# Kernel tuning notes

Measured on AMD Instinct MI355X. Metric: run time of the kernel, lower is better.

Reference implementation:

```python
import jax, jax.numpy as jnp
import numpy as np

B, T, C, H, D, S = 4096, 256, 64, 16, 16, 10


def setup_inputs() -> dict:
    key = jax.random.key(0)
    ks = jax.random.split(key, 8)
    return {
        'states_seq': jax.random.uniform(ks[0], (B, T, S), dtype=jnp.float32) + 0.5,
        'covariates_seq': jax.random.normal(ks[1], (B, T, C), dtype=jnp.float32),
        'ln_gamma': jnp.ones((C,), jnp.float32),
        'ln_beta': jnp.zeros((C,), jnp.float32),
        'rnn_wx': jax.random.normal(ks[2], (C, H), dtype=jnp.float32) * 0.1,
        'rnn_wh': jax.random.normal(ks[3], (H, H), dtype=jnp.float32) * 0.1,
        'rnn_b': jnp.zeros((H,), jnp.float32),
        'd1_w': jax.random.normal(ks[4], (H, H), dtype=jnp.float32) * 0.1,
        'd1_b': jnp.zeros((H,), jnp.float32),
        'd2_w': jax.random.normal(ks[5], (H, D), dtype=jnp.float32) * 0.1,
        'd2_b': jnp.zeros((D,), jnp.float32),
    }


def _cash_budget(s, d):
    # Deterministic cash-budget accounting update.
    # s: (B, 10) = [rev_prev, cash, AR, inventory, PPE, AP, debt, equity, retained, other]
    # d: (B, 16) drivers; first 10 used as ratios.
    sig = jax.nn.sigmoid
    g      = jnp.tanh(d[:, 0]) * 0.2      # sales growth
    cogs_m = sig(d[:, 1])                 # COGS margin
    opex_m = sig(d[:, 2]) * 0.5           # opex margin
    dep_r  = sig(d[:, 3]) * 0.1           # depreciation rate on PPE
    capex_r = sig(d[:, 4]) * 0.2          # capex as % of revenue
    dso = sig(d[:, 5])                    # AR ratio
    dio = sig(d[:, 6])                    # inventory ratio
    dpo = sig(d[:, 7])                    # AP ratio
    tax_r = sig(d[:, 8]) * 0.35           # tax rate
    int_r = sig(d[:, 9]) * 0.1            # interest rate on debt

    rev_prev, cash, ar, inv, ppe, ap, debt, equity, re, other = [s[:, i] for i in range(10)]
    rev = rev_prev * (1.0 + g)
    cogs = cogs_m * rev
    opex = opex_m * rev
    dep = dep_r * ppe
    interest = int_r * debt
    ebt = rev - cogs - opex - dep - interest
    tax = tax_r * jnp.maximum(ebt, 0.0)
    ni = ebt - tax
    ar_new = dso * rev
    inv_new = dio * cogs
    ap_new = dpo * cogs
    capex = capex_r * rev
    ppe_new = ppe + capex - dep
    cash_new = cash + ni + dep - capex - (ar_new - ar) - (inv_new - inv) + (ap_new - ap)
    re_new = re + ni
    s_next = jnp.stack([rev, cash_new, ar_new, inv_new, ppe_new, ap_new, debt, equity, re_new, other], axis=-1)
    is_out = jnp.stack([rev, cogs, opex, dep, interest, tax, ni], axis=-1)  # (B, 7)
    return s_next, is_out


def reference(states_seq, covariates_seq, ln_gamma, ln_beta, rnn_wx, rnn_wh, rnn_b, d1_w, d1_b, d2_w, d2_b):
    # LayerNormalization (keras default eps=1e-3, last axis)
    mu = covariates_seq.mean(-1, keepdims=True)
    var = covariates_seq.var(-1, keepdims=True)
    x = (covariates_seq - mu) * jax.lax.rsqrt(var + 1e-3) * ln_gamma + ln_beta

    # SimpleRNN: h_t = tanh(x_t Wx + h_{t-1} Wh + b), return_sequences
    xw = jnp.einsum('btc,ch->bth', x, rnn_wx) + rnn_b  # precompute input projection

    def rnn_step(h, xt):
        h = jnp.tanh(xt + h @ rnn_wh)
        return h, h

    h0 = jnp.zeros((x.shape[0], rnn_wh.shape[0]), x.dtype)
    _, hs = jax.lax.scan(rnn_step, h0, jnp.swapaxes(xw, 0, 1))  # (T, B, H)
    hs = jnp.swapaxes(hs, 0, 1)  # (B, T, H)

    drivers = jnp.tanh(hs @ d1_w + d1_b) @ d2_w + d2_b  # (B, T, D)

    # Cash-budget recurrence over t = 1 .. T-1
    def cb_step(s_prev, d_t):
        s_next, is_out = _cash_budget(s_prev, d_t)
        return s_next, (s_next, is_out)

    s0 = states_seq[:, 0, :]
    _, (states_tm, is_tm) = jax.lax.scan(cb_step, s0, jnp.swapaxes(drivers[:, 1:, :], 0, 1))
    states_pred = jnp.swapaxes(states_tm, 0, 1)  # (B, T-1, 10)
    is_pred = jnp.swapaxes(is_tm, 0, 1)          # (B, T-1, 7)
    return states_pred, is_pred
```

## Files before the change

kernel.cpp:

```cpp
#include <hip/hip_runtime.h>

#define NB 4096
#define NT 256
#define NC 64
#define NH 16
#define NS 10
#define NTO 255

__device__ __forceinline__ float fast_rcp(float x){
#if __has_builtin(__builtin_amdgcn_rcpf)
    return __builtin_amdgcn_rcpf(x);
#else
    return 1.0f/x;
#endif
}
__device__ __forceinline__ float fast_rsq(float x){
#if __has_builtin(__builtin_amdgcn_rsqf)
    return __builtin_amdgcn_rsqf(x);
#else
    return rsqrtf(x);
#endif
}
__device__ __forceinline__ float fsig(float x){
    return fast_rcp(1.0f + __expf(-x));
}
__device__ __forceinline__ float ftanh(float x){
    float e = __expf(2.0f*x);
    return fmaf(-2.0f, fast_rcp(e + 1.0f), 1.0f);
}

__global__ __launch_bounds__(64, 1) void vpf_kernel(
    const float* __restrict__ states, const float* __restrict__ cov,
    const float* __restrict__ lng,    const float* __restrict__ lnb,
    const float* __restrict__ wx,     const float* __restrict__ wh,
    const float* __restrict__ rnb,    const float* __restrict__ d1w,
    const float* __restrict__ d1b,    const float* __restrict__ d2w,
    const float* __restrict__ d2b,    float* __restrict__ out)
{
    const int lane = threadIdx.x;
    const int g = lane >> 4, l = lane & 15;
    const int b = (blockIdx.x << 2) + g;

    __shared__ __align__(16) float buf[2][4*NC];

    float gw[NC]; float Gs = 0.f, bacc = 0.f;
    #pragma unroll
    for (int c = 0; c < NC; ++c) {
        float w = wx[c*NH + l];
        float t = lng[c] * w;
        gw[c] = t; Gs += t;
        bacc = fmaf(lnb[c], w, bacc);
    }
    const float bwb = bacc + rnb[l];
    float whc[NH], d1c[NH], d2c[NH];
    #pragma unroll
    for (int k = 0; k < NH; ++k) {
        whc[k] = wh[k*NH + l];
        d1c[k] = d1w[k*NH + l];
        d2c[k] = d2w[k*NH + l];
    }
    const float d1bl = d1b[l], d2bl = d2b[l];

    float s0,s1,s2,s3,s4,s5,s6,s7,s8,s9;
    { const float* sp = states + (size_t)b*NT*NS;
      s0=sp[0];s1=sp[1];s2=sp[2];s3=sp[3];s4=sp[4];
      s5=sp[5];s6=sp[6];s7=sp[7];s8=sp[8];s9=sp[9]; }

    float* spo = out + (size_t)b*NTO*NS + l;
    float* ipo = out + (size_t)NB*NTO*NS + (size_t)b*NTO*7 + l;

    const float4* gp = (const float4*)(cov + (size_t)b*NT*NC) + l;
    float4 v0 = gp[0];
    float4 v1 = gp[16];
    float4 ra = gp[32];
    float4 rb = gp[48];
    ((float4*)buf[0])[lane] = v0;
    ((float4*)buf[1])[lane] = v1;
    __syncthreads();

    auto compute_xw = [&](const float* bp) -> float {
        const float4* row = (const float4*)(bp + g*NC);
        float4 ov = row[l];
        float ss = (ov.x+ov.y)+(ov.z+ov.w);
        float sq = fmaf(ov.x,ov.x, fmaf(ov.y,ov.y, fmaf(ov.z,ov.z, ov.w*ov.w)));
        #pragma unroll
        for (int m = 1; m < 16; m <<= 1) {
            ss += __shfl_xor(ss, m);
            sq += __shfl_xor(sq, m);
        }
        float mu  = ss * (1.0f/64.0f);
        float var = fmaf(-mu, mu, sq * (1.0f/64.0f));
        float rs  = fast_rsq(var + 0.001f);
        float a0=0.f, a1=0.f, a2=0.f, a3=0.f;
        #pragma unroll
        for (int c = 0; c < 16; ++c) {
            float4 v = row[c];
            a0 = fmaf(v.x, gw[4*c+0], a0);
            a1 = fmaf(v.y, gw[4*c+1], a1);
            a2 = fmaf(v.z, gw[4*c+2], a2);
            a3 = fmaf(v.w, gw[4*c+3], a3);
        }
        float dot = (a0+a1)+(a2+a3);
        return fmaf(rs, fmaf(-mu, Gs, dot), bwb);
    };

    float xw = compute_xw(buf[0]);
    float hrep[NH];
    #pragma unroll
    for (int j = 0; j < NH; ++j) hrep[j] = 0.f;
    const int base4 = (lane & 48) << 2;

    #pragma unroll 1
    for (int t = 0; t < NT; ++t) {
        if (t < NT-2) { ((float4*)buf[t&1])[lane] = ra; ra = rb; }
        if (t < NT-4) { rb = gp[(t+4)*16]; }
        float xwn = 0.f;
        if (t < NT-1) xwn = compute_xw(buf[(t+1)&1]);

        float a0 = xw, a1 = 0.f;
        #pragma unroll
        for (int k = 0; k < NH; k += 2) {
            a0 = fmaf(hrep[k],   whc[k],   a0);
            a1 = fmaf(hrep[k+1], whc[k+1], a1);
        }
        float hn = ftanh(a0 + a1);
        int hni = __float_as_int(hn);
        #pragma unroll
        for (int j = 0; j < NH; ++j)
            hrep[j] = __int_as_float(__builtin_amdgcn_ds_bpermute(base4 + 4*j, hni));

        if (t >= 1) {
            float b0 = d1bl, b1 = 0.f;
            #pragma unroll
            for (int k = 0; k < NH; k += 2) {
                b0 = fmaf(hrep[k],   d1c[k],   b0);
                b1 = fmaf(hrep[k+1], d1c[k+1], b1);
            }
            float t1 = ftanh(b0 + b1);
            int t1i = __float_as_int(t1);
            float t1rep[NH];
            #pragma unroll
            for (int j = 0; j < NH; ++j)
                t1rep[j] = __int_as_float(__builtin_amdgcn_ds_bpermute(base4 + 4*j, t1i));
            float c0 = d2bl, c1 = 0.f;
            #pragma unroll
            for (int k = 0; k < NH; k += 2) {
                c0 = fmaf(t1rep[k],   d2c[k],   c0);
                c1 = fmaf(t1rep[k+1], d2c[k+1], c1);
            }
            float dv = c0 + c1;
            int dvi = __float_as_int(dv);
            float dd[10];
            #pragma unroll
            for (int j = 0; j < 10; ++j)
                dd[j] = __int_as_float(__builtin_amdgcn_ds_bpermute(base4 + 4*j, dvi));

            float gg    = 0.2f  * ftanh(dd[0]);
            float cogsm = fsig(dd[1]);
            float opexm = 0.5f  * fsig(dd[2]);
            float depr  = 0.1f  * fsig(dd[3]);
            float capr  = 0.2f  * fsig(dd[4]);
            float dso   = fsig(dd[5]);
            float dio   = fsig(dd[6]);
            float dpo   = fsig(dd[7]);
            float taxr  = 0.35f * fsig(dd[8]);
            float intr  = 0.1f  * fsig(dd[9]);

            float rev   = fmaf(s0, gg, s0);
            float cogs  = cogsm * rev;
            float opex  = opexm * rev;
            float dep   = depr * s4;
            float inte  = intr * s6;
            float ebt   = (((rev - cogs) - opex) - dep) - inte;
            float tax   = taxr * fmaxf(ebt, 0.0f);
            float ni    = ebt - tax;
            float arn   = dso * rev;
            float invn  = dio * cogs;
            float apn   = dpo * cogs;
            float capex = capr * rev;
            float ppen  = (s4 + capex) - dep;
            float cashn = (((((s1 + ni) + dep) - capex) - (arn - s2)) - (invn - s3)) + (apn - s5);
            float ren   = s8 + ni;

            s0=rev; s1=cashn; s2=arn; s3=invn; s4=ppen; s5=apn; s8=ren;

            float sv = (l==0)?rev:(l==1)?cashn:(l==2)?arn:(l==3)?invn:(l==4)?ppen:
                       (l==5)?apn:(l==6)?s6:(l==7)?s7:(l==8)?ren:s9;
            float iv = (l==0)?rev:(l==1)?cogs:(l==2)?opex:(l==3)?dep:(l==4)?inte:(l==5)?tax:ni;
            if (l < NS) *spo = sv;
            if (l < 7)  *ipo = iv;
            spo += NS; ipo += 7;
        }
        xw = xwn;
        __syncthreads();
    }
}

extern "C" void kernel_launch(void* const* d_in, const int* in_sizes, int n_in,
                              void* d_out, int out_size, void* d_ws, size_t ws_size,
                              hipStream_t stream) {
    (void)in_sizes; (void)n_in; (void)d_ws; (void)ws_size; (void)out_size;
    vpf_kernel<<<NB/4, 64, 0, stream>>>(
        (const float*)d_in[0],
        (const float*)d_in[1],
        (const float*)d_in[2],
        (const float*)d_in[3],
        (const float*)d_in[4],
        (const float*)d_in[5],
        (const float*)d_in[6],
        (const float*)d_in[7],
        (const float*)d_in[8],
        (const float*)d_in[9],
        (const float*)d_in[10],
        (float*)d_out);
}
```

Baseline: 685.7 us.

## Precompute input projections into LDS as fp16, then run lean recurrence loop

Splits the kernel into two phases. The first computes all LayerNorm+input-projection values up front and stores them in shared memory as packed half2. The second runs the serial RNN and cash-budget recurrence, reading those values back, which removes the per-step normalisation work and the barrier from the dependent chain. Broadcasts now go through LDS stores and float4 loads instead of per-element bpermute, and the ten driver activations are computed one per lane via a tanh-as-sigmoid identity and read back with vector loads. Storing the projections in fp16 loses precision. Dropping barriers depends on wavefront-synchronous LDS behaviour within the single 64-lane block. The large shared array also raises LDS use per block.

```diff
diff --git a/kernel.cpp b/kernel.cpp
--- a/kernel.cpp
+++ b/kernel.cpp
@@ -1,4 +1,5 @@
 #include <hip/hip_runtime.h>
+#include <hip/hip_fp16.h>
 
 #define NB 4096
 #define NT 256
@@ -41,7 +42,11 @@
     const int g = lane >> 4, l = lane & 15;
     const int b = (blockIdx.x << 2) + g;
 
-    __shared__ __align__(16) float buf[2][4*NC];
+    __shared__ __half2 xws[128*64];
+    __shared__ __align__(16) float stg[2][4*NC];
+    __shared__ __align__(16) float hb[64];
+    __shared__ __align__(16) float tb[64];
+    __shared__ __align__(16) float db[64];
 
     float gw[NC]; float Gs = 0.f, bacc = 0.f;
     #pragma unroll
@@ -60,23 +65,9 @@
         d2c[k] = d2w[k*NH + l];
     }
     const float d1bl = d1b[l], d2bl = d2b[l];
-
-    float s0,s1,s2,s3,s4,s5,s6,s7,s8,s9;
-    { const float* sp = states + (size_t)b*NT*NS;
-      s0=sp[0];s1=sp[1];s2=sp[2];s3=sp[3];s4=sp[4];
-      s5=sp[5];s6=sp[6];s7=sp[7];s8=sp[8];s9=sp[9]; }
-
-    float* spo = out + (size_t)b*NTO*NS + l;
-    float* ipo = out + (size_t)NB*NTO*NS + (size_t)b*NTO*7 + l;
-
-    const float4* gp = (const float4*)(cov + (size_t)b*NT*NC) + l;
-    float4 v0 = gp[0];
-    float4 v1 = gp[16];
-    float4 ra = gp[32];
-    float4 rb = gp[48];
-    ((float4*)buf[0])[lane] = v0;
-    ((float4*)buf[1])[lane] = v1;
-    __syncthreads();
+    const float Aa = (l==0)?0.4f:(l==2)?0.5f:(l==3)?0.1f:(l==4)?0.2f:(l==8)?0.35f:(l==9)?0.1f:1.0f;
+    const float Ba = (l==0)?2.0f:1.0f;
+    const float Ca = (l==0)?-0.2f:0.0f;
 
     auto compute_xw = [&](const float* bp) -> float {
         const float4* row = (const float4*)(bp + g*NC);
@@ -104,30 +95,68 @@
         return fmaf(rs, fmaf(-mu, Gs, dot), bwb);
     };
 
-    float xw = compute_xw(buf[0]);
+    const float4* gp = (const float4*)(cov + (size_t)b*NT*NC) + l;
+    float4 ra, rb2, rc, rd;
+    {
+        float4 v0 = gp[0], v1 = gp[16];
+        ra = gp[32]; rb2 = gp[48]; rc = gp[64]; rd = gp[80];
+        ((float4*)stg[0])[lane] = v0;
+        ((float4*)stg[1])[lane] = v1;
+    }
+    float xw_even = 0.f;
+    #pragma unroll 2
+    for (int p = 0; p < NT; ++p) {
+        float xwv = compute_xw(stg[p&1]);
+        if (p < NT-2) ((float4*)stg[p&1])[lane] = ra;
+        ra = rb2; rb2 = rc; rc = rd;
+        if (p < NT-6) rd = gp[(p+6)*16];
+        if (p & 1) {
+            xws[(p>>1)*64 + lane] = __halves2half2(__float2half(xw_even), __float2half(xwv));
+        } else {
+            xw_even = xwv;
+        }
+    }
+
+    float s0,s1,s2,s3,s4,s5,s6,s7,s8,s9;
+    { const float* sp = states + (size_t)b*NT*NS;
+      s0=sp[0];s1=sp[1];s2=sp[2];s3=sp[3];s4=sp[4];
+      s5=sp[5];s6=sp[6];s7=sp[7];s8=sp[8];s9=sp[9]; }
+
+    float* spo = out + (size_t)b*NTO*NS + l;
+    float* ipo = out + (size_t)NB*NTO*NS + (size_t)b*NTO*7 + l;
+
     float hrep[NH];
     #pragma unroll
     for (int j = 0; j < NH; ++j) hrep[j] = 0.f;
-    const int base4 = (lane & 48) << 2;
-
-    #pragma unroll 1
+
+    __half2 xu = xws[lane];
+    __half2 xun = xu;
+
+    #pragma unroll 2
     for (int t = 0; t < NT; ++t) {
-        if (t < NT-2) { ((float4*)buf[t&1])[lane] = ra; ra = rb; }
-        if (t < NT-4) { rb = gp[(t+4)*16]; }
-        float xwn = 0.f;
-        if (t < NT-1) xwn = compute_xw(buf[(t+1)&1]);
-
-        float a0 = xw, a1 = 0.f;
+        float xwv;
+        if ((t & 1) == 0) {
+            xwv = __low2float(xu);
+            if (t + 2 < NT) xun = xws[((t+2)>>1)*64 + lane];
+        } else {
+            xwv = __high2float(xu);
+            xu = xun;
+        }
+
+        float a0 = xwv, a1 = 0.f;
         #pragma unroll
         for (int k = 0; k < NH; k += 2) {
             a0 = fmaf(hrep[k],   whc[k],   a0);
             a1 = fmaf(hrep[k+1], whc[k+1], a1);
         }
         float hn = ftanh(a0 + a1);
-        int hni = __float_as_int(hn);
-        #pragma unroll
-        for (int j = 0; j < NH; ++j)
-            hrep[j] = __int_as_float(__builtin_amdgcn_ds_bpermute(base4 + 4*j, hni));
+        hb[lane] = hn;
+        { const float4* hp = ((const float4*)hb) + g*4;
+          float4 h0 = hp[0], h1 = hp[1], h2 = hp[2], h3 = hp[3];
+          hrep[0]=h0.x; hrep[1]=h0.y; hrep[2]=h0.z; hrep[3]=h0.w;
+          hrep[4]=h1.x; hrep[5]=h1.y; hrep[6]=h1.z; hrep[7]=h1.w;
+          hrep[8]=h2.x; hrep[9]=h2.y; hrep[10]=h2.z; hrep[11]=h2.w;
+          hrep[12]=h3.x; hrep[13]=h3.y; hrep[14]=h3.z; hrep[15]=h3.w; }
 
         if (t >= 1) {
             float b0 = d1bl, b1 = 0.f;
@@ -137,47 +166,42 @@
                 b1 = fmaf(hrep[k+1], d1c[k+1], b1);
             }
             float t1 = ftanh(b0 + b1);
-            int t1i = __float_as_int(t1);
-            float t1rep[NH];
-            #pragma unroll
-            for (int j = 0; j < NH; ++j)
-                t1rep[j] = __int_as_float(__builtin_amdgcn_ds_bpermute(base4 + 4*j, t1i));
+            tb[lane] = t1;
+            float tr[NH];
+            { const float4* tp = ((const float4*)tb) + g*4;
+              float4 u0 = tp[0], u1 = tp[1], u2 = tp[2], u3 = tp[3];
+              tr[0]=u0.x; tr[1]=u0.y; tr[2]=u0.z; tr[3]=u0.w;
+              tr[4]=u1.x; tr[5]=u1.y; tr[6]=u1.z; tr[7]=u1.w;
+              tr[8]=u2.x; tr[9]=u2.y; tr[10]=u2.z; tr[11]=u2.w;
+              tr[12]=u3.x; tr[13]=u3.y; tr[14]=u3.z; tr[15]=u3.w; }
             float c0 = d2bl, c1 = 0.f;
             #pragma unroll
             for (int k = 0; k < NH; k += 2) {
-                c0 = fmaf(t1rep[k],   d2c[k],   c0);
-                c1 = fmaf(t1rep[k+1], d2c[k+1], c1);
+                c0 = fmaf(tr[k],   d2c[k],   c0);
+                c1 = fmaf(tr[k+1], d2c[k+1], c1);
             }
             float dv = c0 + c1;
-            int dvi = __float_as_int(dv);
-            float dd[10];
-            #pragma unroll
-            for (int j = 0; j < 10; ++j)
-                dd[j] = __int_as_float(__builtin_amdgcn_ds_bpermute(base4 + 4*j, dvi));
-
-            float gg    = 0.2f  * ftanh(dd[0]);
-            float cogsm = fsig(dd[1]);
-            float opexm = 0.5f  * fsig(dd[2]);
-            float depr  = 0.1f  * fsig(dd[3]);
-            float capr  = 0.2f  * fsig(dd[4]);
-            float dso   = fsig(dd[5]);
-            float dio   = fsig(dd[6]);
-            float dpo   = fsig(dd[7]);
-            float taxr  = 0.35f * fsig(dd[8]);
-            float intr  = 0.1f  * fsig(dd[9]);
-
-            float rev   = fmaf(s0, gg, s0);
-            float cogs  = cogsm * rev;
-            float opex  = opexm * rev;
-            float dep   = depr * s4;
-            float inte  = intr * s6;
+            float act = fmaf(Aa, fsig(Ba * dv), Ca);
+            db[lane] = act;
+            float dd0,dd1,dd2,dd3,dd4,dd5,dd6,dd7,dd8,dd9;
+            { const float4* dp = ((const float4*)db) + g*4;
+              float4 w0 = dp[0], w1 = dp[1], w2 = dp[2];
+              dd0=w0.x; dd1=w0.y; dd2=w0.z; dd3=w0.w;
+              dd4=w1.x; dd5=w1.y; dd6=w1.z; dd7=w1.w;
+              dd8=w2.x; dd9=w2.y; }
+
+            float rev   = fmaf(s0, dd0, s0);
+            float cogs  = dd1 * rev;
+            float opex  = dd2 * rev;
+            float dep   = dd3 * s4;
+            float inte  = dd9 * s6;
             float ebt   = (((rev - cogs) - opex) - dep) - inte;
-            float tax   = taxr * fmaxf(ebt, 0.0f);
+            float tax   = dd8 * fmaxf(ebt, 0.0f);
             float ni    = ebt - tax;
-            float arn   = dso * rev;
-            float invn  = dio * cogs;
-            float apn   = dpo * cogs;
-            float capex = capr * rev;
+            float arn   = dd5 * rev;
+            float invn  = dd6 * cogs;
+            float apn   = dd7 * cogs;
+            float capex = dd4 * rev;
             float ppen  = (s4 + capex) - dep;
             float cashn = (((((s1 + ni) + dep) - capex) - (arn - s2)) - (invn - s3)) + (apn - s5);
             float ren   = s8 + ni;
@@ -191,8 +215,6 @@
             if (l < 7)  *ipo = iv;
             spo += NS; ipo += 7;
         }
-        xw = xwn;
-        __syncthreads();
     }
 }
 
```

Result: faster. 669.5 us (-2.4%).
